# Kernel optimization log

Measured on AMD Instinct MI355X. Metric: run time of the kernel, lower is better.

Reference implementation:

```python
import jax, jax.numpy as jnp
import numpy as np

BN_EPS = 1e-5


def _fc_bn_relu(x, W, b, gamma, beta):
    # 1x1 conv (channels-last linear) + BatchNorm2d (training-mode batch stats) + ReLU
    y = jnp.einsum('btnc,cd->btnd', x, W) + b
    mu = y.mean(axis=(0, 1, 2), keepdims=True)
    var = y.var(axis=(0, 1, 2), keepdims=True)  # biased var, as torch BN uses for normalization
    y = (y - mu) * jax.lax.rsqrt(var + BN_EPS) * gamma + beta
    return jax.nn.relu(y)


def setup_inputs() -> dict:
    key = jax.random.key(0)
    ks = jax.random.split(key, 8)
    B, Cin, N, T, D = 16, 16, 512, 64, 8  # Cin = 2*D
    x = jax.random.normal(ks[0], (B, Cin, N, T), jnp.float32)

    def lin(k, i, o):
        # xavier-uniform-ish init
        lim = np.sqrt(6.0 / (i + o)).astype(np.float32)
        return jax.random.uniform(k, (i, o), jnp.float32, -lim, lim)

    return {
        'x': x, 'time_ind': 0,
        'Wq': lin(ks[1], Cin, D), 'bq': jnp.zeros(D), 'gq': jnp.ones(D), 'betaq': jnp.zeros(D),
        'Wk': lin(ks[2], Cin, D), 'bk': jnp.zeros(D), 'gk': jnp.ones(D), 'betak': jnp.zeros(D),
        'Wv': lin(ks[3], Cin, D), 'bv': jnp.zeros(D), 'gv': jnp.ones(D), 'betav': jnp.zeros(D),
        'Wo': lin(ks[4], D, 2 * D), 'bo': jnp.zeros(2 * D), 'go': jnp.ones(2 * D), 'betao': jnp.zeros(2 * D),
    }


def reference(x, time_ind, Wq, bq, gq, betaq, Wk, bk, gk, betak, Wv, bv, gv, betav, Wo, bo, go, betao):
    K, d = 2, 4  # torch.split(.., K, dim=-1): head_dim=K=2, n_heads=D/K=d=4
    B = x.shape[0]
    xt = jnp.transpose(x, (0, 3, 2, 1))  # [B, T, N, 2D]
    T, N = xt.shape[1], xt.shape[2]
    q = _fc_bn_relu(xt, Wq, bq, gq, betaq)  # [B, T, N, D]
    k = _fc_bn_relu(xt, Wk, bk, gk, betak)
    v = _fc_bn_relu(xt, Wv, bv, gv, betav)
    H = q.shape[-1] // K  # 4 heads
    q = q.reshape(B, T, N, H, K)
    k = k.reshape(B, T, N, H, K)
    v = v.reshape(B, T, N, H, K)
    # scores: [B, N, H, Tq, Tk]; scale by 1/sqrt(d) per original code
    attn = jnp.einsum('bqnhc,bknhc->bnhqk', q, k) / jnp.sqrt(jnp.float32(d))
    attn = jax.nn.softmax(attn, axis=-1)
    out = jnp.einsum('bnhqk,bknhc->bqnhc', attn, v).reshape(B, T, N, H * K)  # head-major channel concat
    out = _fc_bn_relu(out, Wo, bo, go, betao)  # [B, T, N, 2D]
    return jnp.transpose(out, (0, 3, 2, 1))  # [B, 2D, N, T]
```

## Files before the change

### kernel.cpp

```cpp
#include <hip/hip_runtime.h>
#include <math.h>

#define NPOS      524288
#define CH_STRIDE 32768
#define B_STRIDE  524288
#define BN_EPS    1e-5f
#define INV_NPOS  (1.0f / 524288.0f)
#define LOG2E     1.44269504088896340736f

__device__ __forceinline__ float wave_red64(float v) {
    v += __shfl_xor(v, 32);
    v += __shfl_xor(v, 16);
    v += __shfl_xor(v, 8);
    v += __shfl_xor(v, 4);
    v += __shfl_xor(v, 2);
    v += __shfl_xor(v, 1);
    return v;
}

__device__ __forceinline__ float exp2_fast(float x) {
#if __has_builtin(__builtin_amdgcn_exp2f)
    return __builtin_amdgcn_exp2f(x);
#else
    float r;
    asm volatile("v_exp_f32 %0, %1\n\ts_nop 1" : "=v"(r) : "v"(x));
    return r;
#endif
}

__device__ __forceinline__ float rlane(float v, int lane) {
    return __int_as_float(__builtin_amdgcn_readlane(__float_as_int(v), lane));
}

__global__ __launch_bounds__(256) void stats_qkv_kernel(
    const float* __restrict__ x,
    const float* __restrict__ Wq, const float* __restrict__ bq,
    const float* __restrict__ Wk, const float* __restrict__ bk,
    const float* __restrict__ Wv, const float* __restrict__ bv,
    float* __restrict__ stats )
{
    float acc_s[24], acc_q[24];
#pragma unroll
    for (int j = 0; j < 24; ++j) { acc_s[j] = 0.f; acc_q[j] = 0.f; }

    int t = blockIdx.x * 256 + threadIdx.x;
    int p = t * 4;
    int b = p >> 15;
    int r = p & 32767;
    const float* xb = x + b * B_STRIDE + r;

    float4 xv[16];
#pragma unroll
    for (int c = 0; c < 16; ++c) xv[c] = *(const float4*)(xb + c * CH_STRIDE);

#pragma unroll
    for (int j = 0; j < 8; ++j) {
        float4 yq = make_float4(bq[j], bq[j], bq[j], bq[j]);
        float4 yk = make_float4(bk[j], bk[j], bk[j], bk[j]);
        float4 yv = make_float4(bv[j], bv[j], bv[j], bv[j]);
#pragma unroll
        for (int c = 0; c < 16; ++c) {
            float wq = Wq[c * 8 + j], wk = Wk[c * 8 + j], wv = Wv[c * 8 + j];
            yq.x = fmaf(xv[c].x, wq, yq.x); yq.y = fmaf(xv[c].y, wq, yq.y);
            yq.z = fmaf(xv[c].z, wq, yq.z); yq.w = fmaf(xv[c].w, wq, yq.w);
            yk.x = fmaf(xv[c].x, wk, yk.x); yk.y = fmaf(xv[c].y, wk, yk.y);
            yk.z = fmaf(xv[c].z, wk, yk.z); yk.w = fmaf(xv[c].w, wk, yk.w);
            yv.x = fmaf(xv[c].x, wv, yv.x); yv.y = fmaf(xv[c].y, wv, yv.y);
            yv.z = fmaf(xv[c].z, wv, yv.z); yv.w = fmaf(xv[c].w, wv, yv.w);
        }
        acc_s[j]      += (yq.x + yq.y) + (yq.z + yq.w);
        acc_q[j]      += fmaf(yq.x, yq.x, yq.y * yq.y) + fmaf(yq.z, yq.z, yq.w * yq.w);
        acc_s[8 + j]  += (yk.x + yk.y) + (yk.z + yk.w);
        acc_q[8 + j]  += fmaf(yk.x, yk.x, yk.y * yk.y) + fmaf(yk.z, yk.z, yk.w * yk.w);
        acc_s[16 + j] += (yv.x + yv.y) + (yv.z + yv.w);
        acc_q[16 + j] += fmaf(yv.x, yv.x, yv.y * yv.y) + fmaf(yv.z, yv.z, yv.w * yv.w);
    }

    __shared__ float red[4][48];
    int w = threadIdx.x >> 6, lane = threadIdx.x & 63;
#pragma unroll
    for (int j = 0; j < 24; ++j) {
        float vs = wave_red64(acc_s[j]);
        float vq = wave_red64(acc_q[j]);
        if (lane == 0) { red[w][j] = vs; red[w][24 + j] = vq; }
    }
    __syncthreads();
    if (threadIdx.x < 48) {
        float v = red[0][threadIdx.x] + red[1][threadIdx.x] + red[2][threadIdx.x] + red[3][threadIdx.x];
        atomicAdd(&stats[threadIdx.x], v);
    }
}

__global__ __launch_bounds__(256) void attn_kernel(
    const float* __restrict__ x, const float* __restrict__ stats,
    const float* __restrict__ Wq, const float* __restrict__ bq,
    const float* __restrict__ gq, const float* __restrict__ betaq,
    const float* __restrict__ Wk, const float* __restrict__ bk,
    const float* __restrict__ gk, const float* __restrict__ betak,
    const float* __restrict__ Wv, const float* __restrict__ bv,
    const float* __restrict__ gv, const float* __restrict__ betav,
    float* __restrict__ attnbuf )
{
    __shared__ float effW[24][16];
    __shared__ float effB[24];

    int tid = threadIdx.x;
    if (tid < 24) {
        int grp = tid >> 3, jj = tid & 7;
        const float* W  = (grp == 0) ? Wq : (grp == 1) ? Wk : Wv;
        const float* bb = (grp == 0) ? bq : (grp == 1) ? bk : bv;
        const float* g  = (grp == 0) ? gq : (grp == 1) ? gk : gv;
        const float* be = (grp == 0) ? betaq : (grp == 1) ? betak : betav;
        float mean = stats[tid] * INV_NPOS;
        float var  = stats[24 + tid] * INV_NPOS - mean * mean;
        float s    = g[jj] * rsqrtf(var + BN_EPS);
        float a    = (grp == 0) ? 0.5f * LOG2E : 1.0f;
        float sa   = s * a;
        for (int c = 0; c < 16; ++c) effW[tid][c] = W[c * 8 + jj] * sa;
        effB[tid] = (bb[jj] * s + be[jj] - mean * s) * a;
    }
    __syncthreads();

    int w = tid >> 6, lane = tid & 63;
    int pair = blockIdx.x * 4 + w;
    int b = pair >> 9, n = pair & 511;
    const float* xb = x + b * B_STRIDE + n * 64 + lane;

    float xv[16];
#pragma unroll
    for (int c = 0; c < 16; ++c) xv[c] = xb[c * CH_STRIDE];

    float q[8], kk[8], vv[8];
#pragma unroll
    for (int jj = 0; jj < 8; ++jj) {
        float yq = effB[jj], yk = effB[8 + jj], yv = effB[16 + jj];
        const float4* wq4 = (const float4*)(&effW[jj][0]);
        const float4* wk4 = (const float4*)(&effW[8 + jj][0]);
        const float4* wv4 = (const float4*)(&effW[16 + jj][0]);
#pragma unroll
        for (int c4 = 0; c4 < 4; ++c4) {
            float4 a4 = wq4[c4], b4 = wk4[c4], c4v = wv4[c4];
            yq = fmaf(xv[4*c4+0], a4.x, fmaf(xv[4*c4+1], a4.y, fmaf(xv[4*c4+2], a4.z, fmaf(xv[4*c4+3], a4.w, yq))));
            yk = fmaf(xv[4*c4+0], b4.x, fmaf(xv[4*c4+1], b4.y, fmaf(xv[4*c4+2], b4.z, fmaf(xv[4*c4+3], b4.w, yk))));
            yv = fmaf(xv[4*c4+0], c4v.x, fmaf(xv[4*c4+1], c4v.y, fmaf(xv[4*c4+2], c4v.z, fmaf(xv[4*c4+3], c4v.w, yv))));
        }
        q[jj]  = fmaxf(yq, 0.f);
        kk[jj] = fmaxf(yk, 0.f);
        vv[jj] = fmaxf(yv, 0.f);
    }

    float se[4], o0[4], o1[4];
#pragma unroll
    for (int h = 0; h < 4; ++h) { se[h] = 0.f; o0[h] = 0.f; o1[h] = 0.f; }

#pragma unroll 8
    for (int j = 0; j < 64; ++j) {
#pragma unroll
        for (int h = 0; h < 4; ++h) {
            float k0 = rlane(kk[2*h],     j);
            float k1 = rlane(kk[2*h + 1], j);
            float v0 = rlane(vv[2*h],     j);
            float v1 = rlane(vv[2*h + 1], j);
            float e = exp2_fast(fmaf(q[2*h], k0, q[2*h + 1] * k1));
            se[h] += e;
            o0[h] = fmaf(e, v0, o0[h]);
            o1[h] = fmaf(e, v1, o1[h]);
        }
    }

    float out[8];
#pragma unroll
    for (int h = 0; h < 4; ++h) {
        float inv = 1.0f / se[h];
        out[2*h]     = o0[h] * inv;
        out[2*h + 1] = o1[h] * inv;
    }

    float4* dst = (float4*)(attnbuf + (size_t)pair * 512 + lane * 8);
    dst[0] = make_float4(out[0], out[1], out[2], out[3]);
    dst[1] = make_float4(out[4], out[5], out[6], out[7]);
}

__global__ __launch_bounds__(256) void statsA_kernel(
    const float* __restrict__ attnbuf,
    float* __restrict__ statsA )
{
    float sumA[8], cross[36];
#pragma unroll
    for (int i = 0; i < 8; ++i) sumA[i] = 0.f;
#pragma unroll
    for (int i = 0; i < 36; ++i) cross[i] = 0.f;

    int g = blockIdx.x * 256 + threadIdx.x;
    for (int p = g; p < NPOS; p += 131072) {
        const float4* src = (const float4*)(attnbuf + (size_t)p * 8);
        float4 a0 = src[0], a1 = src[1];
        float a[8] = { a0.x, a0.y, a0.z, a0.w, a1.x, a1.y, a1.z, a1.w };
        int cnt = 0;
#pragma unroll
        for (int i = 0; i < 8; ++i) {
            sumA[i] += a[i];
#pragma unroll
            for (int j = i; j < 8; ++j) { cross[cnt] = fmaf(a[i], a[j], cross[cnt]); ++cnt; }
        }
    }

    __shared__ float red[4][44];
    int w = threadIdx.x >> 6, lane = threadIdx.x & 63;
#pragma unroll
    for (int i = 0; i < 8; ++i) {
        float v = wave_red64(sumA[i]);
        if (lane == 0) red[w][i] = v;
    }
#pragma unroll
    for (int i = 0; i < 36; ++i) {
        float v = wave_red64(cross[i]);
        if (lane == 0) red[w][8 + i] = v;
    }
    __syncthreads();
    if (threadIdx.x < 44) {
        float v = red[0][threadIdx.x] + red[1][threadIdx.x] + red[2][threadIdx.x] + red[3][threadIdx.x];
        atomicAdd(&statsA[threadIdx.x], v);
    }
}

__global__ __launch_bounds__(256) void out_kernel(
    const float* __restrict__ attnbuf, const float* __restrict__ statsA,
    const float* __restrict__ Wo, const float* __restrict__ bo,
    const float* __restrict__ go, const float* __restrict__ betao,
    float* __restrict__ outp)
{
    __shared__ float effWo[16][8];
    __shared__ float effbo[16];

    int tid = threadIdx.x;
    if (tid < 16) {
        int d = tid;
        float mA[8];
#pragma unroll
        for (int i = 0; i < 8; ++i) mA[i] = statsA[i] * INV_NPOS;
        float mean = bo[d];
#pragma unroll
        for (int i = 0; i < 8; ++i) mean = fmaf(mA[i], Wo[i * 16 + d], mean);
        float var = 0.f;
        int cnt = 0;
#pragma unroll
        for (int i = 0; i < 8; ++i) {
#pragma unroll
            for (int j = i; j < 8; ++j) {
                float cov = statsA[8 + cnt] * INV_NPOS - mA[i] * mA[j];
                ++cnt;
                float wterm = Wo[i * 16 + d] * Wo[j * 16 + d];
                var += (i == j) ? wterm * cov : 2.f * wterm * cov;
            }
        }
        float s = go[d] * rsqrtf(var + BN_EPS);
        for (int i = 0; i < 8; ++i) effWo[d][i] = Wo[i * 16 + d] * s;
        effbo[d] = bo[d] * s + betao[d] - mean * s;
    }
    __syncthreads();

    int w = tid >> 6, lane = tid & 63;
    int pair = blockIdx.x * 4 + w;
    int b = pair >> 9, n = pair & 511;

    const float4* src = (const float4*)(attnbuf + (size_t)pair * 512 + lane * 8);
    float4 a0 = src[0], a1 = src[1];
    float a[8] = { a0.x, a0.y, a0.z, a0.w, a1.x, a1.y, a1.z, a1.w };

    float* ob = outp + b * B_STRIDE + n * 64 + lane;
#pragma unroll
    for (int d = 0; d < 16; ++d) {
        const float4* wr = (const float4*)(&effWo[d][0]);
        float4 w0 = wr[0], w1 = wr[1];
        float o = effbo[d];
        o = fmaf(a[0], w0.x, fmaf(a[1], w0.y, fmaf(a[2], w0.z, fmaf(a[3], w0.w, o))));
        o = fmaf(a[4], w1.x, fmaf(a[5], w1.y, fmaf(a[6], w1.z, fmaf(a[7], w1.w, o))));
        ob[d * CH_STRIDE] = fmaxf(o, 0.f);
    }
}

extern "C" void kernel_launch(void* const* d_in, const int* in_sizes, int n_in,
                              void* d_out, int out_size, void* d_ws, size_t ws_size,
                              hipStream_t stream)
{
    const float* x     = (const float*)d_in[0];
    const float* Wq    = (const float*)d_in[2];
    const float* bq    = (const float*)d_in[3];
    const float* gq    = (const float*)d_in[4];
    const float* betaq = (const float*)d_in[5];
    const float* Wk    = (const float*)d_in[6];
    const float* bk    = (const float*)d_in[7];
    const float* gk    = (const float*)d_in[8];
    const float* betak = (const float*)d_in[9];
    const float* Wv    = (const float*)d_in[10];
    const float* bv    = (const float*)d_in[11];
    const float* gv    = (const float*)d_in[12];
    const float* betav = (const float*)d_in[13];
    const float* Wo    = (const float*)d_in[14];
    const float* bo    = (const float*)d_in[15];
    const float* go    = (const float*)d_in[16];
    const float* betao = (const float*)d_in[17];

    float* ws      = (float*)d_ws;
    float* stats   = ws;
    float* statsA  = ws + 48;
    float* attnbuf = ws + 1024;

    hipMemsetAsync(d_ws, 0, 4096, stream);

    stats_qkv_kernel<<<512, 256, 0, stream>>>(x, Wq, bq, Wk, bk, Wv, bv, stats);
    attn_kernel<<<2048, 256, 0, stream>>>(x, stats,
                                          Wq, bq, gq, betaq,
                                          Wk, bk, gk, betak,
                                          Wv, bv, gv, betav,
                                          attnbuf);
    statsA_kernel<<<512, 256, 0, stream>>>(attnbuf, statsA);
    out_kernel<<<2048, 256, 0, stream>>>(attnbuf, statsA, Wo, bo, go, betao, (float*)d_out);
}
```

Baseline: 219.3 us.

## Fuse attention-output statistics into attn kernel and stage K/V via LDS

Removes the separate statsA pass by computing per-channel sums and cross products of the attention output inside attn_kernel. It uses wave reductions and shared-memory atomics, then one global atomic per block. This avoids re-reading the whole attention buffer from memory. K/V broadcasts now go through LDS float4 reads instead of readlane. The fused kernel takes on extra shuffle reduction work per wave.

```diff
diff --git a/kernel.cpp b/kernel.cpp
--- a/kernel.cpp
+++ b/kernel.cpp
@@ -28,10 +28,6 @@
 #endif
 }
 
-__device__ __forceinline__ float rlane(float v, int lane) {
-    return __int_as_float(__builtin_amdgcn_readlane(__float_as_int(v), lane));
-}
-
 __global__ __launch_bounds__(256) void stats_qkv_kernel(
     const float* __restrict__ x,
     const float* __restrict__ Wq, const float* __restrict__ bq,
@@ -99,10 +95,13 @@
     const float* __restrict__ gk, const float* __restrict__ betak,
     const float* __restrict__ Wv, const float* __restrict__ bv,
     const float* __restrict__ gv, const float* __restrict__ betav,
-    float* __restrict__ attnbuf )
+    float* __restrict__ attnbuf ,
+    float* __restrict__ statsA  )
 {
     __shared__ float effW[24][16];
     __shared__ float effB[24];
+    __shared__ float4 kvsh[4][4][64];
+    __shared__ float sA[44];
 
     int tid = threadIdx.x;
     if (tid < 24) {
@@ -119,6 +118,7 @@
         for (int c = 0; c < 16; ++c) effW[tid][c] = W[c * 8 + jj] * sa;
         effB[tid] = (bb[jj] * s + be[jj] - mean * s) * a;
     }
+    if (tid < 44) sA[tid] = 0.f;
     __syncthreads();
 
     int w = tid >> 6, lane = tid & 63;
@@ -149,6 +149,10 @@
         vv[jj] = fmaxf(yv, 0.f);
     }
 
+#pragma unroll
+    for (int h = 0; h < 4; ++h)
+        kvsh[w][h][lane] = make_float4(kk[2*h], kk[2*h+1], vv[2*h], vv[2*h+1]);
+
     float se[4], o0[4], o1[4];
 #pragma unroll
     for (int h = 0; h < 4; ++h) { se[h] = 0.f; o0[h] = 0.f; o1[h] = 0.f; }
@@ -157,14 +161,11 @@
     for (int j = 0; j < 64; ++j) {
 #pragma unroll
         for (int h = 0; h < 4; ++h) {
-            float k0 = rlane(kk[2*h],     j);
-            float k1 = rlane(kk[2*h + 1], j);
-            float v0 = rlane(vv[2*h],     j);
-            float v1 = rlane(vv[2*h + 1], j);
-            float e = exp2_fast(fmaf(q[2*h], k0, q[2*h + 1] * k1));
+            float4 kc = kvsh[w][h][j];
+            float e = exp2_fast(fmaf(q[2*h], kc.x, q[2*h + 1] * kc.y));
             se[h] += e;
-            o0[h] = fmaf(e, v0, o0[h]);
-            o1[h] = fmaf(e, v1, o1[h]);
+            o0[h] = fmaf(e, kc.z, o0[h]);
+            o1[h] = fmaf(e, kc.w, o1[h]);
         }
     }
 
@@ -179,49 +180,26 @@
     float4* dst = (float4*)(attnbuf + (size_t)pair * 512 + lane * 8);
     dst[0] = make_float4(out[0], out[1], out[2], out[3]);
     dst[1] = make_float4(out[4], out[5], out[6], out[7]);
-}
-
-__global__ __launch_bounds__(256) void statsA_kernel(
-    const float* __restrict__ attnbuf,
-    float* __restrict__ statsA )
-{
-    float sumA[8], cross[36];
-#pragma unroll
-    for (int i = 0; i < 8; ++i) sumA[i] = 0.f;
-#pragma unroll
-    for (int i = 0; i < 36; ++i) cross[i] = 0.f;
-
-    int g = blockIdx.x * 256 + threadIdx.x;
-    for (int p = g; p < NPOS; p += 131072) {
-        const float4* src = (const float4*)(attnbuf + (size_t)p * 8);
-        float4 a0 = src[0], a1 = src[1];
-        float a[8] = { a0.x, a0.y, a0.z, a0.w, a1.x, a1.y, a1.z, a1.w };
-        int cnt = 0;
+
+#pragma unroll
+    for (int i = 0; i < 8; ++i) {
+        float t = wave_red64(out[i]);
+        if (lane == 0) atomicAdd(&sA[i], t);
+    }
+    {
+        int cnt = 8;
 #pragma unroll
         for (int i = 0; i < 8; ++i) {
-            sumA[i] += a[i];
-#pragma unroll
-            for (int j = i; j < 8; ++j) { cross[cnt] = fmaf(a[i], a[j], cross[cnt]); ++cnt; }
-        }
-    }
-
-    __shared__ float red[4][44];
-    int w = threadIdx.x >> 6, lane = threadIdx.x & 63;
-#pragma unroll
-    for (int i = 0; i < 8; ++i) {
-        float v = wave_red64(sumA[i]);
-        if (lane == 0) red[w][i] = v;
-    }
-#pragma unroll
-    for (int i = 0; i < 36; ++i) {
-        float v = wave_red64(cross[i]);
-        if (lane == 0) red[w][8 + i] = v;
-    }
-    __syncthreads();
-    if (threadIdx.x < 44) {
-        float v = red[0][threadIdx.x] + red[1][threadIdx.x] + red[2][threadIdx.x] + red[3][threadIdx.x];
-        atomicAdd(&statsA[threadIdx.x], v);
-    }
+#pragma unroll
+            for (int j2 = i; j2 < 8; ++j2) {
+                float t = wave_red64(out[i] * out[j2]);
+                if (lane == 0) atomicAdd(&sA[cnt], t);
+                ++cnt;
+            }
+        }
+    }
+    __syncthreads();
+    if (tid < 44) atomicAdd(&statsA[tid], sA[tid]);
 }
 
 __global__ __launch_bounds__(256) void out_kernel(
@@ -307,14 +285,13 @@
     float* statsA  = ws + 48;
     float* attnbuf = ws + 1024;
 
-    hipMemsetAsync(d_ws, 0, 4096, stream);
+    hipMemsetAsync(d_ws, 0, 512, stream);
 
     stats_qkv_kernel<<<512, 256, 0, stream>>>(x, Wq, bq, Wk, bk, Wv, bv, stats);
     attn_kernel<<<2048, 256, 0, stream>>>(x, stats,
                                           Wq, bq, gq, betaq,
                                           Wk, bk, gk, betak,
                                           Wv, bv, gv, betav,
-                                          attnbuf);
-    statsA_kernel<<<512, 256, 0, stream>>>(attnbuf, statsA);
+                                          attnbuf, statsA);
     out_kernel<<<2048, 256, 0, stream>>>(attnbuf, statsA, Wo, bo, go, betao, (float*)d_out);
 }
```

Result: no change. 216.7 us (-1.2%).
